# Kernel tuning notes

Hardware: AMD Instinct MI355X
Metric: run time of the kernel (lower is better)

Reference implementation:

```python
import jax, jax.numpy as jnp
import numpy as np

K = 3            # kernel size (odd)
CO, CI = 16, 16  # out/in channels

def setup_inputs() -> dict:
    key = jax.random.key(0)
    k1, k2, k3, k4 = jax.random.split(key, 4)
    B, C, H, W = 4, CI, 128, 128
    input_data = jax.random.normal(k1, (B, C, H, W), dtype=jnp.float32)
    # fixation coordinates in pixel units
    foa_xy = jax.random.uniform(k2, (B, 2), dtype=jnp.float32) * jnp.array([W, H], jnp.float32)
    hidden = 256
    W1 = jax.random.normal(k3, (2, hidden), dtype=jnp.float32) * (1.0 / jnp.sqrt(2.0))
    b1 = jnp.zeros((hidden,), jnp.float32)
    W2 = jax.random.normal(k4, (hidden, CO * CI * K * K), dtype=jnp.float32) * (1.0 / jnp.sqrt(hidden))
    b2 = jnp.zeros((CO * CI * K * K,), jnp.float32)
    return {"input_data": input_data, "foa_xy": foa_xy, "W1": W1, "b1": b1, "W2": W2, "b2": b2}

def _unfold_reflect(x, k):
    # x: [B, C, H, W] -> patches [B, C, k*k, H*W], reflect padding, stride 1, dilation 1
    B, C, H, W = x.shape
    pad = (k - 1) // 2
    xp = jnp.pad(x, ((0, 0), (0, 0), (pad, pad), (pad, pad)), mode="reflect")
    rows = [xp[:, :, i:i + H, j:j + W] for i in range(k) for j in range(k)]
    return jnp.stack(rows, axis=2).reshape(B, C, k * k, H * W)

def reference(input_data, foa_xy, W1, b1, W2, b2):
    B, C, H, W = input_data.shape
    # coordinate grid [H*W, 2] as (x, y), matching torch meshgrid(ij) + stack(xx, yy)
    ys = jnp.arange(H, dtype=jnp.float32)
    xs = jnp.arange(W, dtype=jnp.float32)
    yy, xx = jnp.meshgrid(ys, xs, indexing="ij")
    coords = jnp.stack([xx.ravel(), yy.ravel()], axis=1)         # [HW, 2]
    net_in = (coords[None, :, :] - foa_xy[:, None, :]).reshape(B * H * W, 2)
    # kernel-generating MLP
    h = jax.nn.relu(net_in @ W1 + b1)
    net_out = h @ W2 + b2                                        # [B*HW, CO*CI*K*K]
    kernel = net_out.reshape(B, H * W, CO, CI, K * K)            # [B, P, o, i, q]
    patches = _unfold_reflect(input_data, K)                     # [B, CI, K*K, HW]
    # per-pixel conv: sum over in-channels and kernel taps
    out = jnp.einsum("biqp,bpoiq->bop", patches, kernel)         # [B, CO, HW]
    return out.reshape(B, CO, H, W)
```

## Files before the change

### kernel.cpp

```cpp
#include <hip/hip_runtime.h>

#define CI    16
#define CO    16
#define HID   256
#define KPAD  288
#define NKK   9
#define NKH   8
#define NCH   144
#define IMGH  128
#define IMGW  128
#define RSTR  68
#define KKSTR (NCH * 32)
#define OSTRS (NKK * NCH * 32)

typedef float f32x4  __attribute__((ext_vector_type(4)));
typedef float f32x2  __attribute__((ext_vector_type(2)));
typedef short bf16x8 __attribute__((ext_vector_type(8)));

__device__ __host__ __forceinline__ short f2bf(float f) {
  union { float f; unsigned u; } c; c.f = f;
  unsigned b = c.u + 0x7FFFu + ((c.u >> 16) & 1u);
  return (short)(b >> 16);
}

__global__ void prep_w2(const float* __restrict__ W2, const float* __restrict__ b2,
                        short* __restrict__ W2b) {
  __shared__ float tile[32][65];
  const int kk = blockIdx.x % NKK;
  const int colbase = (blockIdx.x / NKK) * 64;
  const int tid = threadIdx.x;

  for (int e = tid; e < 2048; e += 256) {
    int klr = e >> 6;
    int cc  = e & 63;
    int col = colbase + cc;
    float v;
    if (kk < 8) v = W2[(kk * 32 + klr) * (CO * NCH) + col];
    else        v = (klr == 0) ? b2[col] : 0.f;
    tile[klr][cc] = v;
  }
  __syncthreads();
  for (int e = tid; e < 2048; e += 256) {
    int cc = e >> 5;
    int kl = e & 31;
    int col = colbase + cc;
    int o = col / NCH;
    int n = col - o * NCH;
    int i = n / 9, q = n - i * 9;
    int dyr = q / 3, dx = q - dyr * 3;
    int np = dx * 48 + i * 3 + dyr;
    W2b[(((o * NKK + kk) * NCH + np) << 5) + kl] = f2bf(tile[kl][cc]);
  }
}

__global__ __launch_bounds__(256, 4)
void ngconv_main(const float* __restrict__ in, const float* __restrict__ foa,
                 const float* __restrict__ W1, const float* __restrict__ b1,
                 const short* __restrict__ W2b, float* __restrict__ out) {
  __shared__ short shHf[32 * 512];
  __shared__ short shPatch[48 * RSTR];

  const int tid  = threadIdx.x;
  const int lane = tid & 63;
  const int wv   = tid >> 6;
  const int c15  = lane & 15;
  const int quad = lane >> 4;

  const int blk = blockIdx.x;
  const int b   = blk >> 8;
  const int rem = blk & 255;
  const int y   = rem >> 1;
  const int x0  = (rem & 1) << 6;

  const float fx  = foa[b * 2 + 0];
  const float fy  = foa[b * 2 + 1];
  const float dyv = (float)y - fy;

  const int ry0 = (y == 0) ? 1 : (y - 1);
  const int ry2 = (y == IMGH - 1) ? (IMGH - 2) : (y + 1);

  for (int e = tid; e < 48 * 66; e += 256) {
    int r  = e / 66;
    int xx = e - r * 66;
    int i = r / 3, dyr = r - i * 3;
    int ryr = (dyr == 0) ? ry0 : ((dyr == 1) ? y : ry2);
    int x = x0 + xx - 1;
    x = (x < 0) ? 1 : ((x > IMGW - 1) ? (IMGW - 2) : x);
    shPatch[r * RSTR + xx] = f2bf(in[((b * CI + i) * IMGH + ryr) * IMGW + x]);
  }

  for (int g = tid; g < 64 * 32; g += 256) {
    int px = g & 63;
    int ks = g >> 6;
    int k0 = ks << 3;
    float dxv = (float)(x0 + px) - fx;
    short hv[8];
    #pragma unroll
    for (int j = 0; j < 8; ++j) {
      int k = k0 + j;
      float h = fmaxf(fmaf(dxv, W1[k], fmaf(dyv, W1[HID + k], b1[k])), 0.f);
      hv[j] = f2bf(h);
    }
    int ms = px >> 4;
    int kk = k0 >> 5;
    int lslot = ((k0 & 31) >> 3) * 16 + (px & 15);
    *(bf16x8*)&shHf[((ms * NKH + kk) << 9) + (lslot << 3)] = *(bf16x8*)hv;
  }

  bf16x8 af8 = (bf16x8){0, 0, 0, 0, 0, 0, 0, 0};
  if (quad == 0) af8[0] = (short)0x3F80;

  __syncthreads();

  #pragma unroll 1
  for (int oj = 0; oj < 4; ++oj) {
    const int o = wv + oj * 4;
    const short* Bo = W2b + o * OSTRS + (c15 << 5) + (quad << 3);

    f32x2 P2[8];
    #pragma unroll
    for (int t = 0; t < 8; ++t) P2[t] = (f32x2){0.f, 0.f};

    #pragma unroll 1
    for (int pass = 0; pass < 3; ++pass) {
      const short* Bp = Bo + (pass * 3) * 512;
      f32x4 acc[4][3];
      #pragma unroll
      for (int ms = 0; ms < 4; ++ms)
        #pragma unroll
        for (int j = 0; j < 3; ++j)
          acc[ms][j] = (f32x4){0.f, 0.f, 0.f, 0.f};

      bf16x8 bE[3], bO[3];
      #pragma unroll
      for (int j = 0; j < 3; ++j) bE[j] = *(const bf16x8*)&Bp[j << 9];

      #pragma unroll 1
      for (int t = 0; t < 4; ++t) {
        const int kkE = 2 * t;
        #pragma unroll
        for (int j = 0; j < 3; ++j)
          bO[j] = *(const bf16x8*)&Bp[(kkE + 1) * KKSTR + (j << 9)];
        {
          const short* hp = shHf + (kkE << 9) + (lane << 3);
          #pragma unroll
          for (int ms = 0; ms < 4; ++ms) {
            bf16x8 af = *(const bf16x8*)&hp[ms * (NKH << 9)];
            #pragma unroll
            for (int j = 0; j < 3; ++j)
              acc[ms][j] = __builtin_amdgcn_mfma_f32_16x16x32_bf16(
                  af, bE[j], acc[ms][j], 0, 0, 0);
          }
        }
        #pragma unroll
        for (int j = 0; j < 3; ++j)
          bE[j] = *(const bf16x8*)&Bp[(kkE + 2) * KKSTR + (j << 9)];
        {
          const short* hp = shHf + ((kkE + 1) << 9) + (lane << 3);
          #pragma unroll
          for (int ms = 0; ms < 4; ++ms) {
            bf16x8 af = *(const bf16x8*)&hp[ms * (NKH << 9)];
            #pragma unroll
            for (int j = 0; j < 3; ++j)
              acc[ms][j] = __builtin_amdgcn_mfma_f32_16x16x32_bf16(
                  af, bO[j], acc[ms][j], 0, 0, 0);
          }
        }
      }
      {
        #pragma unroll
        for (int ms = 0; ms < 4; ++ms)
          #pragma unroll
          for (int j = 0; j < 3; ++j)
            acc[ms][j] = __builtin_amdgcn_mfma_f32_16x16x32_bf16(
                af8, bE[j], acc[ms][j], 0, 0, 0);
      }

      const int sh = pass << 4;
      #pragma unroll
      for (int j = 0; j < 3; ++j) {
        const short* prow = &shPatch[((j << 4) + c15) * RSTR + (quad << 2)];
        #pragma unroll
        for (int ms = 0; ms < 4; ++ms) {
          uint2 u0 = *(const uint2*)&prow[ms * 16];
          unsigned u1 = *(const unsigned*)&prow[ms * 16 + 4];
          unsigned long long a0 =
              (unsigned long long)u0.x | ((unsigned long long)u0.y << 32);
          unsigned long long a1 =
              (unsigned long long)u0.y | ((unsigned long long)u1 << 32);
          unsigned d0 = (unsigned)(a0 >> sh);
          unsigned d1 = (unsigned)(a1 >> sh);
          float p0 = __uint_as_float(d0 << 16);
          float p1 = __uint_as_float(d0 & 0xFFFF0000u);
          float p2 = __uint_as_float(d1 << 16);
          float p3 = __uint_as_float(d1 & 0xFFFF0000u);
          f32x2 a01 = {acc[ms][j][0], acc[ms][j][1]};
          f32x2 a23 = {acc[ms][j][2], acc[ms][j][3]};
          P2[ms * 2 + 0] += a01 * (f32x2){p0, p1};
          P2[ms * 2 + 1] += a23 * (f32x2){p2, p3};
        }
      }
    }

    float P[16];
    #pragma unroll
    for (int t = 0; t < 16; ++t) P[t] = P2[t >> 1][t & 1];
    #pragma unroll
    for (int m = 8; m >= 1; m >>= 1) {
      const bool hi = (c15 & m) != 0;
      #pragma unroll
      for (int j = 0; j < m; ++j) {
        float keep = hi ? P[j + m] : P[j];
        float send = hi ? P[j] : P[j + m];
        float recv = __shfl_xor(send, m, 64);
        P[j] = keep + recv;
      }
    }

    const int x = x0 + (c15 >> 2) * 16 + quad * 4 + (c15 & 3);
    out[((b * CO + o) * IMGH + y) * IMGW + x] = P[0];
  }
}

extern "C" void kernel_launch(void* const* d_in, const int* in_sizes, int n_in,
                              void* d_out, int out_size, void* d_ws, size_t ws_size,
                              hipStream_t stream) {
  const float* in  = (const float*)d_in[0];
  const float* foa = (const float*)d_in[1];
  const float* W1  = (const float*)d_in[2];
  const float* b1  = (const float*)d_in[3];
  const float* W2  = (const float*)d_in[4];
  const float* b2  = (const float*)d_in[5];
  float* out = (float*)d_out;
  short* W2b = (short*)d_ws;

  prep_w2<<<324, 256, 0, stream>>>(W2, b2, W2b);
  ngconv_main<<<1024, 256, 0, stream>>>(in, foa, W1, b1, W2b, out);
}
```

Baseline: 189.9 us.

## Process a full 128-pixel row per block to double reuse of W2 fragments

Each block now covers a whole image row (128 pixels, 8 M-subtiles) instead of half a row. This halves the grid to 512 blocks and doubles the hidden-activation and patch shared-memory buffers. Every W2 bf16 fragment loaded from global memory now feeds twice as many MFMAs, roughly halving W2 traffic per output. In exchange, the accumulator register count doubles, launch bounds drop to 2 blocks per SIMD-group, and fewer blocks are available to fill the CUs.

```diff
diff --git a/kernel.cpp b/kernel.cpp
--- a/kernel.cpp
+++ b/kernel.cpp
@@ -9,7 +9,9 @@
 #define NCH   144
 #define IMGH  128
 #define IMGW  128
-#define RSTR  68
+#define NMS   8
+#define RSTR  132
+#define RLEN  130
 #define KKSTR (NCH * 32)
 #define OSTRS (NKK * NCH * 32)
 
@@ -53,11 +55,11 @@
   }
 }
 
-__global__ __launch_bounds__(256, 4)
+__global__ __launch_bounds__(256, 2)
 void ngconv_main(const float* __restrict__ in, const float* __restrict__ foa,
                  const float* __restrict__ W1, const float* __restrict__ b1,
                  const short* __restrict__ W2b, float* __restrict__ out) {
-  __shared__ short shHf[32 * 512];
+  __shared__ short shHf[64 * 512];
   __shared__ short shPatch[48 * RSTR];
 
   const int tid  = threadIdx.x;
@@ -67,10 +69,8 @@
   const int quad = lane >> 4;
 
   const int blk = blockIdx.x;
-  const int b   = blk >> 8;
-  const int rem = blk & 255;
-  const int y   = rem >> 1;
-  const int x0  = (rem & 1) << 6;
+  const int b   = blk >> 7;
+  const int y   = blk & 127;
 
   const float fx  = foa[b * 2 + 0];
   const float fy  = foa[b * 2 + 1];
@@ -79,21 +79,21 @@
   const int ry0 = (y == 0) ? 1 : (y - 1);
   const int ry2 = (y == IMGH - 1) ? (IMGH - 2) : (y + 1);
 
-  for (int e = tid; e < 48 * 66; e += 256) {
-    int r  = e / 66;
-    int xx = e - r * 66;
+  for (int e = tid; e < 48 * RLEN; e += 256) {
+    int r  = e / RLEN;
+    int xx = e - r * RLEN;
     int i = r / 3, dyr = r - i * 3;
     int ryr = (dyr == 0) ? ry0 : ((dyr == 1) ? y : ry2);
-    int x = x0 + xx - 1;
+    int x = xx - 1;
     x = (x < 0) ? 1 : ((x > IMGW - 1) ? (IMGW - 2) : x);
     shPatch[r * RSTR + xx] = f2bf(in[((b * CI + i) * IMGH + ryr) * IMGW + x]);
   }
 
-  for (int g = tid; g < 64 * 32; g += 256) {
-    int px = g & 63;
-    int ks = g >> 6;
+  for (int g = tid; g < 128 * 32; g += 256) {
+    int px = g & 127;
+    int ks = g >> 7;
     int k0 = ks << 3;
-    float dxv = (float)(x0 + px) - fx;
+    float dxv = (float)px - fx;
     short hv[8];
     #pragma unroll
     for (int j = 0; j < 8; ++j) {
@@ -117,16 +117,16 @@
     const int o = wv + oj * 4;
     const short* Bo = W2b + o * OSTRS + (c15 << 5) + (quad << 3);
 
-    f32x2 P2[8];
+    f32x2 P2[16];
     #pragma unroll
-    for (int t = 0; t < 8; ++t) P2[t] = (f32x2){0.f, 0.f};
+    for (int t = 0; t < 16; ++t) P2[t] = (f32x2){0.f, 0.f};
 
     #pragma unroll 1
     for (int pass = 0; pass < 3; ++pass) {
       const short* Bp = Bo + (pass * 3) * 512;
-      f32x4 acc[4][3];
-      #pragma unroll
-      for (int ms = 0; ms < 4; ++ms)
+      f32x4 acc[NMS][3];
+      #pragma unroll
+      for (int ms = 0; ms < NMS; ++ms)
         #pragma unroll
         for (int j = 0; j < 3; ++j)
           acc[ms][j] = (f32x4){0.f, 0.f, 0.f, 0.f};
@@ -144,7 +144,7 @@
         {
           const short* hp = shHf + (kkE << 9) + (lane << 3);
           #pragma unroll
-          for (int ms = 0; ms < 4; ++ms) {
+          for (int ms = 0; ms < NMS; ++ms) {
             bf16x8 af = *(const bf16x8*)&hp[ms * (NKH << 9)];
             #pragma unroll
             for (int j = 0; j < 3; ++j)
@@ -158,7 +158,7 @@
         {
           const short* hp = shHf + ((kkE + 1) << 9) + (lane << 3);
           #pragma unroll
-          for (int ms = 0; ms < 4; ++ms) {
+          for (int ms = 0; ms < NMS; ++ms) {
             bf16x8 af = *(const bf16x8*)&hp[ms * (NKH << 9)];
             #pragma unroll
             for (int j = 0; j < 3; ++j)
@@ -169,7 +169,7 @@
       }
       {
         #pragma unroll
-        for (int ms = 0; ms < 4; ++ms)
+        for (int ms = 0; ms < NMS; ++ms)
           #pragma unroll
           for (int j = 0; j < 3; ++j)
             acc[ms][j] = __builtin_amdgcn_mfma_f32_16x16x32_bf16(
@@ -181,7 +181,7 @@
       for (int j = 0; j < 3; ++j) {
         const short* prow = &shPatch[((j << 4) + c15) * RSTR + (quad << 2)];
         #pragma unroll
-        for (int ms = 0; ms < 4; ++ms) {
+        for (int ms = 0; ms < NMS; ++ms) {
           uint2 u0 = *(const uint2*)&prow[ms * 16];
           unsigned u1 = *(const unsigned*)&prow[ms * 16 + 4];
           unsigned long long a0 =
@@ -202,23 +202,25 @@
       }
     }
 
-    float P[16];
     #pragma unroll
-    for (int t = 0; t < 16; ++t) P[t] = P2[t >> 1][t & 1];
-    #pragma unroll
-    for (int m = 8; m >= 1; m >>= 1) {
-      const bool hi = (c15 & m) != 0;
-      #pragma unroll
-      for (int j = 0; j < m; ++j) {
-        float keep = hi ? P[j + m] : P[j];
-        float send = hi ? P[j] : P[j + m];
-        float recv = __shfl_xor(send, m, 64);
-        P[j] = keep + recv;
-      }
+    for (int half = 0; half < 2; ++half) {
+      float P[16];
+      #pragma unroll
+      for (int t = 0; t < 16; ++t) P[t] = P2[half * 8 + (t >> 1)][t & 1];
+      #pragma unroll
+      for (int m = 8; m >= 1; m >>= 1) {
+        const bool hi = (c15 & m) != 0;
+        #pragma unroll
+        for (int j = 0; j < m; ++j) {
+          float keep = hi ? P[j + m] : P[j];
+          float send = hi ? P[j] : P[j + m];
+          float recv = __shfl_xor(send, m, 64);
+          P[j] = keep + recv;
+        }
+      }
+      const int x = half * 64 + (c15 >> 2) * 16 + quad * 4 + (c15 & 3);
+      out[((b * CO + o) * IMGH + y) * IMGW + x] = P[0];
     }
-
-    const int x = x0 + (c15 >> 2) * 16 + quad * 4 + (c15 & 3);
-    out[((b * CO + o) * IMGH + y) * IMGW + x] = P[0];
   }
 }
 
@@ -235,5 +237,5 @@
   short* W2b = (short*)d_ws;
 
   prep_w2<<<324, 256, 0, stream>>>(W2, b2, W2b);
-  ngconv_main<<<1024, 256, 0, stream>>>(in, foa, W1, b1, W2b, out);
-}
+  ngconv_main<<<512, 256, 0, stream>>>(in, foa, W1, b1, W2b, out);
+}
```

After: 155.8 us. -18.0%, faster.
